# Kernel tuning notes

Measured on AMD Instinct MI355X. Metric: run time of the kernel, lower is better.

Reference implementation:

```python
import math
import jax, jax.numpy as jnp
import numpy as np

HEAD_DIM = 64
CAUSAL = True


def setup_inputs() -> dict:
    key = jax.random.key(0)
    kq, kk, kv = jax.random.split(key, 3)
    q = jax.random.normal(kq, (2, 16, 1024, HEAD_DIM), dtype=jnp.float32)
    k = jax.random.normal(kk, (2, 16, 8192, HEAD_DIM), dtype=jnp.float32)
    v = jax.random.normal(kv, (2, 16, 8192, HEAD_DIM), dtype=jnp.float32)
    return {"q": q, "k": k, "v": v, "q_chunk_start": 7168}


def reference(q, k, v, q_chunk_start):
    # q: (B, nh, Tq, dh); k, v: (B, nh, Tk, dh)
    Tq = q.shape[2]
    Tk = k.shape[2]
    scale = math.sqrt(HEAD_DIM)
    # scores: (B, nh, Tq, Tk)
    scores = jnp.einsum("bhqd,bhkd->bhqk", q, k) / scale
    if CAUSAL:
        q_pos = jnp.arange(Tq) + q_chunk_start          # (Tq,)
        k_pos = jnp.arange(Tk)                          # (Tk,)
        mask = k_pos[None, :] > q_pos[:, None]          # (Tq, Tk) True = masked
        scores = jnp.where(mask, -jnp.inf, scores)
    attn = jax.nn.softmax(scores, axis=-1)
    attn = jnp.nan_to_num(attn, nan=0.0)                # fully-masked rows -> 0
    return jnp.einsum("bhqk,bhkd->bhqd", attn, v)
```

## Files before the change

kernel.cpp:

```cpp
#include <hip/hip_runtime.h>
#include <hip/hip_bf16.h>

#define TQ 1024
#define TK 8192
#define DH 64
#define NBH 32
#define QT 64
#define KT 64
#define NW 4
#define NTILE (TK / KT)
#define TILE_E (KT * DH)

typedef __attribute__((ext_vector_type(8))) short short8;
typedef __attribute__((ext_vector_type(4))) short short4v;
typedef __attribute__((ext_vector_type(4))) float f32x4;

static __device__ __forceinline__ short f2bf(float f) {
  __hip_bfloat16 h = __float2bfloat16(f);
  return __builtin_bit_cast(short, h);
}

#define GLD16(gsrc, ldst)                                                     \
  __builtin_amdgcn_global_load_lds(                                           \
      (const __attribute__((address_space(1))) unsigned int*)(gsrc),          \
      (__attribute__((address_space(3))) unsigned int*)(ldst), 16, 0, 0)

__global__ __launch_bounds__(256)
void prep(const float* __restrict__ kg, const float* __restrict__ vg,
          short* __restrict__ Kg2, short* __restrict__ Vg2)
{
  __shared__ __align__(16) short Ki[TILE_E];
  __shared__ __align__(16) short Vi[TILE_E];
  const int bid = blockIdx.x;
  const int h = bid >> 7, t = bid & (NTILE - 1);
  const int tid = threadIdx.x;
  const int t_key = tid >> 4;
  const int t_d   = (tid & 15) * 4;

  const float* kp = kg + ((size_t)h * TK + (size_t)t * KT) * DH;
  const float* vp = vg + ((size_t)h * TK + (size_t)t * KT) * DH;

  #pragma unroll
  for (int it = 0; it < 4; ++it) {
    const int key = t_key + it * 16;
    float4 kv = *(const float4*)(kp + key * DH + t_d);
    short4v ks;
    ks[0] = f2bf(kv.x); ks[1] = f2bf(kv.y); ks[2] = f2bf(kv.z); ks[3] = f2bf(kv.w);
    *(short4v*)(&Ki[(key * 64 + t_d) ^ ((key & 7) << 3)]) = ks;

    float4 vv = *(const float4*)(vp + key * DH + t_d);
    Vi[((t_d + 0) * 64 + key) ^ (((t_d + 0) & 7) << 3)] = f2bf(vv.x);
    Vi[((t_d + 1) * 64 + key) ^ (((t_d + 1) & 7) << 3)] = f2bf(vv.y);
    Vi[((t_d + 2) * 64 + key) ^ (((t_d + 2) & 7) << 3)] = f2bf(vv.z);
    Vi[((t_d + 3) * 64 + key) ^ (((t_d + 3) & 7) << 3)] = f2bf(vv.w);
  }
  __syncthreads();

  const size_t base = (size_t)bid * TILE_E;
  *(short8*)(&Kg2[base + tid * 16])     = *(short8*)(&Ki[tid * 16]);
  *(short8*)(&Kg2[base + tid * 16 + 8]) = *(short8*)(&Ki[tid * 16 + 8]);
  *(short8*)(&Vg2[base + tid * 16])     = *(short8*)(&Vi[tid * 16]);
  *(short8*)(&Vg2[base + tid * 16 + 8]) = *(short8*)(&Vi[tid * 16 + 8]);
}

__global__ __launch_bounds__(256, 2)
void attn_main(const float* __restrict__ qg,
               const short* __restrict__ Kg2,
               const short* __restrict__ Vg2,
               const int* __restrict__ qcs_p,
               float* __restrict__ outg)
{
  __shared__ __align__(16) short Kb[2][TILE_E];
  __shared__ __align__(16) short Vb[2][TILE_E];
  __shared__ __align__(16) short Plds[NW][16 * KT];

  const int tid  = threadIdx.x;
  const int wave = tid >> 6;
  const int lane = tid & 63;
  const int lg   = lane >> 4;
  const int li   = lane & 15;

  const int bid = blockIdx.x;
  const int bh  = bid & (NBH - 1);
  const int qt  = bid >> 5;
  const int qcs = *qcs_p;

  const int q_base = qt * QT;
  const int wrow   = wave * 16;

  const float* qp = qg + ((size_t)bh * TQ + q_base + wrow) * DH;
  const size_t tile_base0 = (size_t)bh * NTILE * TILE_E;

  const float qscale = 0.125f * 1.44269504088896f;
  short8 qf[2];
  #pragma unroll
  for (int h = 0; h < 2; ++h) {
    const float* src = qp + li * DH + h * 32 + lg * 8;
    float4 a = *(const float4*)(src);
    float4 b = *(const float4*)(src + 4);
    short8 f;
    f[0] = f2bf(a.x * qscale); f[1] = f2bf(a.y * qscale);
    f[2] = f2bf(a.z * qscale); f[3] = f2bf(a.w * qscale);
    f[4] = f2bf(b.x * qscale); f[5] = f2bf(b.y * qscale);
    f[6] = f2bf(b.z * qscale); f[7] = f2bf(b.w * qscale);
    qf[h] = f;
  }

  f32x4 o[4];
  #pragma unroll
  for (int ct = 0; ct < 4; ++ct) o[ct] = (f32x4){0.f, 0.f, 0.f, 0.f};
  float rm[4], rl[4];
  #pragma unroll
  for (int r = 0; r < 4; ++r) { rm[r] = -1e30f; rl[r] = 0.f; }

  const int lim    = qcs + q_base + QT;
  const int n_keys = lim < TK ? lim : TK;
  const int n_tiles = (n_keys + KT - 1) / KT;

  const int chunk = wave * 2;

  auto stage = [&](int b, int tile) {
    const size_t tb = tile_base0 + (size_t)tile * TILE_E;
    GLD16(Kg2 + tb + (chunk + 0) * 512 + lane * 8, &Kb[b][(chunk + 0) * 512]);
    GLD16(Kg2 + tb + (chunk + 1) * 512 + lane * 8, &Kb[b][(chunk + 1) * 512]);
    GLD16(Vg2 + tb + (chunk + 0) * 512 + lane * 8, &Vb[b][(chunk + 0) * 512]);
    GLD16(Vg2 + tb + (chunk + 1) * 512 + lane * 8, &Vb[b][(chunk + 1) * 512]);
  };

  stage(0, 0);
  __syncthreads();
  int buf = 0;

  for (int tile = 0; tile < n_tiles; ++tile) {
    const int kt0 = tile * KT;
    if (tile + 1 < n_tiles) stage(buf ^ 1, tile + 1);

    f32x4 sv[4];
    __builtin_amdgcn_s_setprio(1);
    #pragma unroll
    for (int t = 0; t < 4; ++t) {
      f32x4 acc = (f32x4){0.f, 0.f, 0.f, 0.f};
      #pragma unroll
      for (int h = 0; h < 2; ++h) {
        int e = ((t * 16 + li) * 64 + h * 32 + lg * 8) ^ ((li & 7) << 3);
        short8 kf = *(const short8*)(&Kb[buf][e]);
        acc = __builtin_amdgcn_mfma_f32_16x16x32_bf16(qf[h], kf, acc, 0, 0, 0);
      }
      sv[t] = acc;
    }
    __builtin_amdgcn_s_setprio(0);

    if (kt0 + KT - 1 > qcs + q_base + wrow) {
      #pragma unroll
      for (int t = 0; t < 4; ++t) {
        const int keyg = kt0 + t * 16 + li;
        #pragma unroll
        for (int r = 0; r < 4; ++r) {
          const int qpos = qcs + q_base + wrow + lg * 4 + r;
          if (keyg > qpos) sv[t][r] = -INFINITY;
        }
      }
    }

    float al[4], mn[4];
    #pragma unroll
    for (int r = 0; r < 4; ++r) {
      float tm = fmaxf(fmaxf(sv[0][r], sv[1][r]), fmaxf(sv[2][r], sv[3][r]));
      #pragma unroll
      for (int off = 1; off < 16; off <<= 1)
        tm = fmaxf(tm, __shfl_xor(tm, off, 64));
      float m2 = fmaxf(rm[r], tm);
      al[r] = __builtin_amdgcn_exp2f(rm[r] - m2);
      mn[r] = m2;
      rm[r] = m2;
    }

    float ps[4] = {0.f, 0.f, 0.f, 0.f};
    #pragma unroll
    for (int t = 0; t < 4; ++t) {
      #pragma unroll
      for (int r = 0; r < 4; ++r) {
        float p = __builtin_amdgcn_exp2f(sv[t][r] - mn[r]);
        ps[r] += p;
        const int row = lg * 4 + r;
        Plds[wave][(row * KT + t * 16 + li) ^ ((row & 7) << 3)] = f2bf(p);
      }
    }

    #pragma unroll
    for (int r = 0; r < 4; ++r) {
      float sum = ps[r];
      #pragma unroll
      for (int off = 1; off < 16; off <<= 1)
        sum += __shfl_xor(sum, off, 64);
      rl[r] = rl[r] * al[r] + sum;
      #pragma unroll
      for (int ct = 0; ct < 4; ++ct) o[ct][r] *= al[r];
    }

    #pragma unroll
    for (int sk = 0; sk < 2; ++sk) {
      int ep = (li * KT + sk * 32 + lg * 8) ^ ((li & 7) << 3);
      short8 pf = *(const short8*)(&Plds[wave][ep]);
      __builtin_amdgcn_s_setprio(1);
      #pragma unroll
      for (int ct = 0; ct < 4; ++ct) {
        int e = ((ct * 16 + li) * 64 + sk * 32 + lg * 8) ^ ((li & 7) << 3);
        short8 vf = *(const short8*)(&Vb[buf][e]);
        o[ct] = __builtin_amdgcn_mfma_f32_16x16x32_bf16(pf, vf, o[ct], 0, 0, 0);
      }
      __builtin_amdgcn_s_setprio(0);
    }

    __syncthreads();
    buf ^= 1;
  }

  float* op = outg + ((size_t)bh * TQ + q_base + wrow) * DH;
  #pragma unroll
  for (int r = 0; r < 4; ++r) {
    const float inv = rl[r] > 0.f ? 1.0f / rl[r] : 0.f;
    #pragma unroll
    for (int ct = 0; ct < 4; ++ct)
      op[(lg * 4 + r) * DH + ct * 16 + li] = o[ct][r] * inv;
  }
}

__global__ __launch_bounds__(256, 2)
void attn_fallback(const float* __restrict__ qg,
                   const float* __restrict__ kg,
                   const float* __restrict__ vg,
                   const int* __restrict__ qcs_p,
                   float* __restrict__ outg)
{
  __shared__ __align__(16) short Klds[KT * DH];
  __shared__ __align__(16) short Vt[DH * KT];
  __shared__ __align__(16) short Plds[NW][16 * KT];

  const int tid  = threadIdx.x;
  const int wave = tid >> 6;
  const int lane = tid & 63;
  const int lg   = lane >> 4;
  const int li   = lane & 15;

  const int bid = blockIdx.x;
  const int bh  = bid & (NBH - 1);
  const int qt  = bid >> 5;
  const int qcs = *qcs_p;

  const int q_base = qt * QT;
  const int wrow   = wave * 16;

  const float* qp = qg + ((size_t)bh * TQ + q_base + wrow) * DH;
  const float* kp = kg + (size_t)bh * TK * DH;
  const float* vp = vg + (size_t)bh * TK * DH;

  const float qscale = 0.125f * 1.44269504088896f;
  short8 qf[2];
  #pragma unroll
  for (int h = 0; h < 2; ++h) {
    const float* src = qp + li * DH + h * 32 + lg * 8;
    float4 a = *(const float4*)(src);
    float4 b = *(const float4*)(src + 4);
    short8 f;
    f[0] = f2bf(a.x * qscale); f[1] = f2bf(a.y * qscale);
    f[2] = f2bf(a.z * qscale); f[3] = f2bf(a.w * qscale);
    f[4] = f2bf(b.x * qscale); f[5] = f2bf(b.y * qscale);
    f[6] = f2bf(b.z * qscale); f[7] = f2bf(b.w * qscale);
    qf[h] = f;
  }

  f32x4 o[4];
  #pragma unroll
  for (int ct = 0; ct < 4; ++ct) o[ct] = (f32x4){0.f, 0.f, 0.f, 0.f};
  float rm[4], rl[4];
  #pragma unroll
  for (int r = 0; r < 4; ++r) { rm[r] = -1e30f; rl[r] = 0.f; }

  const int lim    = qcs + q_base + QT;
  const int n_keys = lim < TK ? lim : TK;
  const int n_tiles = (n_keys + KT - 1) / KT;

  const int t_key = tid >> 4;
  const int t_d   = (tid & 15) * 4;

  for (int tile = 0; tile < n_tiles; ++tile) {
    const int kt0 = tile * KT;
    #pragma unroll
    for (int it = 0; it < 4; ++it) {
      const int key = t_key + it * 16;
      const size_t goff = (size_t)(kt0 + key) * DH + t_d;
      float4 kv = *(const float4*)(kp + goff);
      short4v ks;
      ks[0] = f2bf(kv.x); ks[1] = f2bf(kv.y); ks[2] = f2bf(kv.z); ks[3] = f2bf(kv.w);
      *(short4v*)(&Klds[(key * DH + t_d) ^ ((key & 7) << 3)]) = ks;

      float4 vv = *(const float4*)(vp + goff);
      Vt[((t_d + 0) * KT + key) ^ ((((t_d + 0) >> 1) & 7) << 3)] = f2bf(vv.x);
      Vt[((t_d + 1) * KT + key) ^ ((((t_d + 1) >> 1) & 7) << 3)] = f2bf(vv.y);
      Vt[((t_d + 2) * KT + key) ^ ((((t_d + 2) >> 1) & 7) << 3)] = f2bf(vv.z);
      Vt[((t_d + 3) * KT + key) ^ ((((t_d + 3) >> 1) & 7) << 3)] = f2bf(vv.w);
    }
    __syncthreads();

    f32x4 sv[4];
    #pragma unroll
    for (int t = 0; t < 4; ++t) {
      f32x4 acc = (f32x4){0.f, 0.f, 0.f, 0.f};
      #pragma unroll
      for (int h = 0; h < 2; ++h) {
        int e = ((t * 16 + li) * DH + h * 32 + lg * 8) ^ ((li & 7) << 3);
        short8 kf = *(const short8*)(&Klds[e]);
        acc = __builtin_amdgcn_mfma_f32_16x16x32_bf16(qf[h], kf, acc, 0, 0, 0);
      }
      sv[t] = acc;
    }

    if (kt0 + KT - 1 > qcs + q_base + wrow) {
      #pragma unroll
      for (int t = 0; t < 4; ++t) {
        const int keyg = kt0 + t * 16 + li;
        #pragma unroll
        for (int r = 0; r < 4; ++r) {
          const int qpos = qcs + q_base + wrow + lg * 4 + r;
          if (keyg > qpos) sv[t][r] = -INFINITY;
        }
      }
    }

    float al[4], mn[4];
    #pragma unroll
    for (int r = 0; r < 4; ++r) {
      float tm = fmaxf(fmaxf(sv[0][r], sv[1][r]), fmaxf(sv[2][r], sv[3][r]));
      #pragma unroll
      for (int off = 1; off < 16; off <<= 1)
        tm = fmaxf(tm, __shfl_xor(tm, off, 64));
      float m2 = fmaxf(rm[r], tm);
      al[r] = __builtin_amdgcn_exp2f(rm[r] - m2);
      mn[r] = m2;
      rm[r] = m2;
    }

    float ps[4] = {0.f, 0.f, 0.f, 0.f};
    #pragma unroll
    for (int t = 0; t < 4; ++t) {
      #pragma unroll
      for (int r = 0; r < 4; ++r) {
        float p = __builtin_amdgcn_exp2f(sv[t][r] - mn[r]);
        ps[r] += p;
        const int row = lg * 4 + r;
        Plds[wave][(row * KT + t * 16 + li) ^ ((row & 7) << 3)] = f2bf(p);
      }
    }

    #pragma unroll
    for (int r = 0; r < 4; ++r) {
      float sum = ps[r];
      #pragma unroll
      for (int off = 1; off < 16; off <<= 1)
        sum += __shfl_xor(sum, off, 64);
      rl[r] = rl[r] * al[r] + sum;
      #pragma unroll
      for (int ct = 0; ct < 4; ++ct) o[ct][r] *= al[r];
    }

    #pragma unroll
    for (int sk = 0; sk < 2; ++sk) {
      int ep = (li * KT + sk * 32 + lg * 8) ^ ((li & 7) << 3);
      short8 pf = *(const short8*)(&Plds[wave][ep]);
      #pragma unroll
      for (int ct = 0; ct < 4; ++ct) {
        int d = ct * 16 + li;
        int ev = (d * KT + sk * 32 + lg * 8) ^ (((d >> 1) & 7) << 3);
        short8 vf = *(const short8*)(&Vt[ev]);
        o[ct] = __builtin_amdgcn_mfma_f32_16x16x32_bf16(pf, vf, o[ct], 0, 0, 0);
      }
    }
    __syncthreads();
  }

  float* op = outg + ((size_t)bh * TQ + q_base + wrow) * DH;
  #pragma unroll
  for (int r = 0; r < 4; ++r) {
    const float inv = rl[r] > 0.f ? 1.0f / rl[r] : 0.f;
    #pragma unroll
    for (int ct = 0; ct < 4; ++ct)
      op[(lg * 4 + r) * DH + ct * 16 + li] = o[ct][r] * inv;
  }
}

extern "C" void kernel_launch(void* const* d_in, const int* in_sizes, int n_in,
                              void* d_out, int out_size, void* d_ws, size_t ws_size,
                              hipStream_t stream) {
  const float* q   = (const float*)d_in[0];
  const float* k   = (const float*)d_in[1];
  const float* v   = (const float*)d_in[2];
  const int*   qcs = (const int*)d_in[3];
  float* out = (float*)d_out;

  constexpr size_t IMG_ELEMS = (size_t)NBH * NTILE * TILE_E;
  constexpr size_t WS_NEED   = 2 * IMG_ELEMS * sizeof(short);

  if (ws_size >= WS_NEED) {
    short* Kg2 = (short*)d_ws;
    short* Vg2 = Kg2 + IMG_ELEMS;
    prep<<<dim3(NBH * NTILE), dim3(256), 0, stream>>>(k, v, Kg2, Vg2);
    attn_main<<<dim3(NBH * (TQ / QT)), dim3(256), 0, stream>>>(q, Kg2, Vg2, qcs, out);
  } else {
    attn_fallback<<<dim3(NBH * (TQ / QT)), dim3(256), 0, stream>>>(q, k, v, qcs, out);
  }
}
```

Measured before the change: 383.0 us.

## Split key range across two blocks with partial softmax combine, rewrite prep

```diff
diff --git a/kernel.cpp b/kernel.cpp
--- a/kernel.cpp
+++ b/kernel.cpp
@@ -10,6 +10,7 @@
 #define NW 4
 #define NTILE (TK / KT)
 #define TILE_E (KT * DH)
+#define ROWS (NBH * TQ)
 
 typedef __attribute__((ext_vector_type(8))) short short8;
 typedef __attribute__((ext_vector_type(4))) short short4v;
@@ -29,46 +30,50 @@
 void prep(const float* __restrict__ kg, const float* __restrict__ vg,
           short* __restrict__ Kg2, short* __restrict__ Vg2)
 {
-  __shared__ __align__(16) short Ki[TILE_E];
-  __shared__ __align__(16) short Vi[TILE_E];
   const int bid = blockIdx.x;
   const int h = bid >> 7, t = bid & (NTILE - 1);
   const int tid = threadIdx.x;
-  const int t_key = tid >> 4;
-  const int t_d   = (tid & 15) * 4;
+  const int kq = tid >> 4;
+  const int dq = tid & 15;
 
   const float* kp = kg + ((size_t)h * TK + (size_t)t * KT) * DH;
   const float* vp = vg + ((size_t)h * TK + (size_t)t * KT) * DH;
-
-  #pragma unroll
-  for (int it = 0; it < 4; ++it) {
-    const int key = t_key + it * 16;
-    float4 kv = *(const float4*)(kp + key * DH + t_d);
+  const size_t base = (size_t)bid * TILE_E;
+
+  #pragma unroll
+  for (int j = 0; j < 4; ++j) {
+    const int key = 4 * kq + j;
+    float4 kv = *(const float4*)(kp + key * DH + 4 * dq);
     short4v ks;
     ks[0] = f2bf(kv.x); ks[1] = f2bf(kv.y); ks[2] = f2bf(kv.z); ks[3] = f2bf(kv.w);
-    *(short4v*)(&Ki[(key * 64 + t_d) ^ ((key & 7) << 3)]) = ks;
-
-    float4 vv = *(const float4*)(vp + key * DH + t_d);
-    Vi[((t_d + 0) * 64 + key) ^ (((t_d + 0) & 7) << 3)] = f2bf(vv.x);
-    Vi[((t_d + 1) * 64 + key) ^ (((t_d + 1) & 7) << 3)] = f2bf(vv.y);
-    Vi[((t_d + 2) * 64 + key) ^ (((t_d + 2) & 7) << 3)] = f2bf(vv.z);
-    Vi[((t_d + 3) * 64 + key) ^ (((t_d + 3) & 7) << 3)] = f2bf(vv.w);
-  }
-  __syncthreads();
-
-  const size_t base = (size_t)bid * TILE_E;
-  *(short8*)(&Kg2[base + tid * 16])     = *(short8*)(&Ki[tid * 16]);
-  *(short8*)(&Kg2[base + tid * 16 + 8]) = *(short8*)(&Ki[tid * 16 + 8]);
-  *(short8*)(&Vg2[base + tid * 16])     = *(short8*)(&Vi[tid * 16]);
-  *(short8*)(&Vg2[base + tid * 16 + 8]) = *(short8*)(&Vi[tid * 16 + 8]);
-}
-
-__global__ __launch_bounds__(256, 2)
+    *(short4v*)(&Kg2[base + ((key * 64 + 4 * dq) ^ ((key & 7) << 3))]) = ks;
+  }
+
+  float4 v0 = *(const float4*)(vp + (4 * kq + 0) * DH + 4 * dq);
+  float4 v1 = *(const float4*)(vp + (4 * kq + 1) * DH + 4 * dq);
+  float4 v2 = *(const float4*)(vp + (4 * kq + 2) * DH + 4 * dq);
+  float4 v3 = *(const float4*)(vp + (4 * kq + 3) * DH + 4 * dq);
+  #pragma unroll
+  for (int i = 0; i < 4; ++i) {
+    const int d = 4 * dq + i;
+    short4v vs;
+    vs[0] = f2bf(((const float*)&v0)[i]);
+    vs[1] = f2bf(((const float*)&v1)[i]);
+    vs[2] = f2bf(((const float*)&v2)[i]);
+    vs[3] = f2bf(((const float*)&v3)[i]);
+    *(short4v*)(&Vg2[base + ((d * 64 + 4 * kq) ^ ((d & 7) << 3))]) = vs;
+  }
+}
+
+template<int NS, bool PART>
+__global__ __launch_bounds__(256, (NS == 2 ? 4 : 2))
 void attn_main(const float* __restrict__ qg,
                const short* __restrict__ Kg2,
                const short* __restrict__ Vg2,
                const int* __restrict__ qcs_p,
-               float* __restrict__ outg)
+               float* __restrict__ outg,
+               float* __restrict__ mpart,
+               float* __restrict__ lpart)
 {
   __shared__ __align__(16) short Kb[2][TILE_E];
   __shared__ __align__(16) short Vb[2][TILE_E];
@@ -82,14 +87,17 @@
 
   const int bid = blockIdx.x;
   const int bh  = bid & (NBH - 1);
-  const int qt  = bid >> 5;
+  const int s   = (bid >> 5) & (NS - 1);
+  const int qt  = bid >> (NS == 2 ? 6 : 5);
   const int qcs = *qcs_p;
 
   const int q_base = qt * QT;
   const int wrow   = wave * 16;
+  const int chunk_start = s * (TK / NS);
 
   const float* qp = qg + ((size_t)bh * TQ + q_base + wrow) * DH;
   const size_t tile_base0 = (size_t)bh * NTILE * TILE_E;
+  const int gt0 = chunk_start / KT;
 
   const float qscale = 0.125f * 1.44269504088896f;
   short8 qf[2];
@@ -113,14 +121,15 @@
   #pragma unroll
   for (int r = 0; r < 4; ++r) { rm[r] = -1e30f; rl[r] = 0.f; }
 
-  const int lim    = qcs + q_base + QT;
-  const int n_keys = lim < TK ? lim : TK;
-  const int n_tiles = (n_keys + KT - 1) / KT;
+  int lim = qcs + q_base + QT;
+  if (lim > TK) lim = TK;
+  if (lim > chunk_start + TK / NS) lim = chunk_start + TK / NS;
+  const int n_tiles = (lim - chunk_start + KT - 1) / KT;
 
   const int chunk = wave * 2;
 
-  auto stage = [&](int b, int tile) {
-    const size_t tb = tile_base0 + (size_t)tile * TILE_E;
+  auto stage = [&](int b, int lt) {
+    const size_t tb = tile_base0 + (size_t)(gt0 + lt) * TILE_E;
     GLD16(Kg2 + tb + (chunk + 0) * 512 + lane * 8, &Kb[b][(chunk + 0) * 512]);
     GLD16(Kg2 + tb + (chunk + 1) * 512 + lane * 8, &Kb[b][(chunk + 1) * 512]);
     GLD16(Vg2 + tb + (chunk + 0) * 512 + lane * 8, &Vb[b][(chunk + 0) * 512]);
@@ -131,9 +140,9 @@
   __syncthreads();
   int buf = 0;
 
-  for (int tile = 0; tile < n_tiles; ++tile) {
-    const int kt0 = tile * KT;
-    if (tile + 1 < n_tiles) stage(buf ^ 1, tile + 1);
+  for (int lt = 0; lt < n_tiles; ++lt) {
+    const int kt0 = chunk_start + lt * KT;
+    if (lt + 1 < n_tiles) stage(buf ^ 1, lt + 1);
 
     f32x4 sv[4];
     __builtin_amdgcn_s_setprio(1);
@@ -216,14 +225,58 @@
     buf ^= 1;
   }
 
-  float* op = outg + ((size_t)bh * TQ + q_base + wrow) * DH;
-  #pragma unroll
-  for (int r = 0; r < 4; ++r) {
-    const float inv = rl[r] > 0.f ? 1.0f / rl[r] : 0.f;
-    #pragma unroll
-    for (int ct = 0; ct < 4; ++ct)
-      op[(lg * 4 + r) * DH + ct * 16 + li] = o[ct][r] * inv;
-  }
+  if constexpr (PART) {
+    const size_t rbase = ((size_t)s * NBH + bh) * TQ + q_base + wrow;
+    float* opr = outg + rbase * DH;
+    #pragma unroll
+    for (int r = 0; r < 4; ++r) {
+      #pragma unroll
+      for (int ct = 0; ct < 4; ++ct)
+        opr[(lg * 4 + r) * DH + ct * 16 + li] = o[ct][r];
+      if (li == 0) {
+        mpart[rbase + lg * 4 + r] = rm[r];
+        lpart[rbase + lg * 4 + r] = rl[r];
+      }
+    }
+  } else {
+    float* op = outg + ((size_t)bh * TQ + q_base + wrow) * DH;
+    #pragma unroll
+    for (int r = 0; r < 4; ++r) {
+      const float inv = rl[r] > 0.f ? 1.0f / rl[r] : 0.f;
+      #pragma unroll
+      for (int ct = 0; ct < 4; ++ct)
+        op[(lg * 4 + r) * DH + ct * 16 + li] = o[ct][r] * inv;
+    }
+  }
+}
+
+template<int NS>
+__global__ __launch_bounds__(256)
+void combine(const float* __restrict__ opart,
+             const float* __restrict__ mp,
+             const float* __restrict__ lp,
+             float* __restrict__ outg)
+{
+  const int gid = blockIdx.x * 256 + threadIdx.x;
+  const int rg = gid >> 6;
+  const int d  = gid & 63;
+
+  float m[NS], l[NS];
+  float M = -1e30f;
+  #pragma unroll
+  for (int s = 0; s < NS; ++s) {
+    m[s] = mp[(size_t)s * ROWS + rg];
+    l[s] = lp[(size_t)s * ROWS + rg];
+    M = fmaxf(M, m[s]);
+  }
+  float L = 0.f, acc = 0.f;
+  #pragma unroll
+  for (int s = 0; s < NS; ++s) {
+    float w = __builtin_amdgcn_exp2f(m[s] - M);
+    L += w * l[s];
+    acc += w * opart[((size_t)s * ROWS + rg) * DH + d];
+  }
+  outg[(size_t)rg * DH + d] = L > 0.f ? acc / L : 0.f;
 }
 
 __global__ __launch_bounds__(256, 2)
@@ -398,14 +451,29 @@
   const int*   qcs = (const int*)d_in[3];
   float* out = (float*)d_out;
 
+  constexpr int    NS = 2;
   constexpr size_t IMG_ELEMS = (size_t)NBH * NTILE * TILE_E;
-  constexpr size_t WS_NEED   = 2 * IMG_ELEMS * sizeof(short);
-
-  if (ws_size >= WS_NEED) {
+  constexpr size_t WS_IMG    = 2 * IMG_ELEMS * sizeof(short);
+  constexpr size_t O_ELEMS   = (size_t)NS * ROWS * DH;
+  constexpr size_t ML_ELEMS  = (size_t)NS * ROWS;
+  constexpr size_t WS_FULL   = WS_IMG + (O_ELEMS + 2 * ML_ELEMS) * sizeof(float);
+
+  if (ws_size >= WS_FULL) {
+    short* Kg2 = (short*)d_ws;
+    short* Vg2 = Kg2 + IMG_ELEMS;
+    float* opart = (float*)(Vg2 + IMG_ELEMS);
+    float* mpart = opart + O_ELEMS;
+    float* lpart = mpart + ML_ELEMS;
+    prep<<<dim3(NBH * NTILE), dim3(256), 0, stream>>>(k, v, Kg2, Vg2);
+    attn_main<NS, true><<<dim3(NBH * NS * (TQ / QT)), dim3(256), 0, stream>>>(
+        q, Kg2, Vg2, qcs, opart, mpart, lpart);
+    combine<NS><<<dim3(ROWS * DH / 256), dim3(256), 0, stream>>>(opart, mpart, lpart, out);
+  } else if (ws_size >= WS_IMG) {
     short* Kg2 = (short*)d_ws;
     short* Vg2 = Kg2 + IMG_ELEMS;
     prep<<<dim3(NBH * NTILE), dim3(256), 0, stream>>>(k, v, Kg2, Vg2);
-    attn_main<<<dim3(NBH * (TQ / QT)), dim3(256), 0, stream>>>(q, Kg2, Vg2, qcs, out);
+    attn_main<1, false><<<dim3(NBH * (TQ / QT)), dim3(256), 0, stream>>>(
+        q, Kg2, Vg2, qcs, out, nullptr, nullptr);
   } else {
     attn_fallback<<<dim3(NBH * (TQ / QT)), dim3(256), 0, stream>>>(q, k, v, qcs, out);
   }
```

New measurement: 363.3 us. -5.1%, faster.
